# Kernel optimization log

Hardware: AMD Instinct MI355X
Metric: run time of the kernel (lower is better)

Reference implementation:

```python
import jax, jax.numpy as jnp
import numpy as np

EPS = 1e-5
K = 20  # hardcoded neighborhood size in get_graph_feature / get_neighbors


def _bn(x, p):
    # inference-mode BatchNorm; p = [gamma, beta, running_mean, running_var], channel axis = 1
    g, b, m, v = p
    sh = (1, -1) + (1,) * (x.ndim - 2)
    return (x - m.reshape(sh)) * (g.reshape(sh) / jnp.sqrt(v.reshape(sh) + EPS)) + b.reshape(sh)


def _knn(x, k):
    # x: [B, C, N] -> idx [B, N, k] of nearest neighbors (argmax of -squared-distance)
    xx = jnp.sum(x * x, axis=1)                       # [B, N]
    d = 2.0 * jnp.einsum('bcn,bcm->bnm', x, x) - xx[:, :, None] - xx[:, None, :]
    return jax.lax.top_k(d, k)[1]


def _gather(x, idx):
    # x: [B, C, N], idx: [B, N, k] -> [B, N, k, C]
    xt = jnp.transpose(x, (0, 2, 1))
    b = jnp.arange(x.shape[0])[:, None, None]
    return xt[b, idx]


def _graph_feature(x, k):
    # EdgeConv feature: cat(neighbor, center, center - neighbor) -> [B, 3C, N, k]
    nb = _gather(x, _knn(x, k))                                   # [B, N, k, C]
    xe = jnp.broadcast_to(jnp.transpose(x, (0, 2, 1))[:, :, None, :], nb.shape)
    feat = jnp.concatenate([nb, xe, xe - nb], axis=3)
    return jnp.transpose(feat, (0, 3, 1, 2))


def _att_pool(x, bn_p, w, b):
    # x: [B, C, N, K]; softmax attention over neighbor axis, weighted sum -> [B, C, N]
    h = jax.nn.relu(_bn(x, bn_p))
    att = jnp.einsum('oc,bcnk->bonk', w, h) + b[None, :, None, None]
    return jnp.sum(x * jax.nn.softmax(att, axis=-1), axis=-1)


def _lafe(x, w1, b1, w2, b2, w3, b3):
    # local_attention_extration; x: [B, 3, N] -> [B, 16, N]
    nb = _gather(x, _knn(x, K))                                   # [B, N, K, 3]
    xc = jnp.broadcast_to(jnp.transpose(x, (0, 2, 1))[:, :, None, :], nb.shape)
    xn = xc - nb                                                  # center - neighbor
    nf = jnp.einsum('oc,bnkc->bnko', w1, xc) + b1                 # conv2d1 -> [B,N,K,16]
    sa = jnp.einsum('o,bnko->bnk', w3[0], nf) + b3[0]             # self attention logits
    ef = jnp.einsum('oc,bnkc->bnko', w2, xn) + b2                 # conv2d2 edge feature
    na = jnp.einsum('o,bnko->bnk', w3[0], ef) + b3[0]             # neighbor attention logits
    coefs = jax.nn.softmax(jax.nn.leaky_relu(sa + na, 0.01), axis=-1)  # [B,N,K]
    vals = jnp.einsum('bnk,bnko->bno', coefs, ef)                 # [B,N,16]
    return jnp.transpose(jax.nn.elu(vals), (0, 2, 1))             # [B,16,N]


def _mk_bn(key, c):
    k1, k2, k3, k4 = jax.random.split(key, 4)
    g = 1.0 + 0.1 * jax.random.normal(k1, (c,))
    be = 0.1 * jax.random.normal(k2, (c,))
    m = 0.1 * jax.random.normal(k3, (c,))
    v = jax.random.uniform(k4, (c,), minval=0.5, maxval=1.5)
    return jnp.stack([g, be, m, v])


def setup_inputs() -> dict:
    key = jax.random.key(0)
    ks = jax.random.split(key, 20)
    B, N, E = 8, 2048, 512
    s = 0.05
    inp = {
        'x': jax.random.normal(ks[0], (B, 3, N), dtype=jnp.float32),
        'la_w1': s * jax.random.normal(ks[1], (16, 3)),
        'la_b1': s * jax.random.normal(ks[2], (16,)),
        'la_w2': s * jax.random.normal(ks[3], (16, 3)),
        'la_b2': s * jax.random.normal(ks[4], (16,)),
        'la_w3': s * jax.random.normal(ks[5], (1, 16)),
        'la_b3': s * jax.random.normal(ks[6], (1,)),
        'mlp_w': s * jax.random.normal(ks[7], (256, 19)),
        'mlp_b': s * jax.random.normal(ks[8], (256,)),
        'mlp_bn': _mk_bn(ks[9], 256),
        'w1': s * jax.random.normal(ks[10], (64, 57)),
        'bn1': _mk_bn(ks[11], 64),
        'w2': s * jax.random.normal(ks[12], (256, 249)),
        'bn2': _mk_bn(ks[13], 256),
        'w3': s * jax.random.normal(ks[14], (E, 512)),
        'bn3': _mk_bn(ks[15], E),
        'p1_bn': _mk_bn(ks[16], 64),
        'p1_w': s * jax.random.normal(ks[17], (64, 64)),
        'p1_b': s * jax.random.normal(ks[17], (64,)),
        'p2_bn': _mk_bn(ks[18], 256),
        'p2_w': s * jax.random.normal(ks[19], (256, 256)),
        'p2_b': s * jax.random.normal(ks[19], (256,)),
    }
    return inp


def reference(x, la_w1, la_b1, la_w2, la_b2, la_w3, la_b3,
              mlp_w, mlp_b, mlp_bn, w1, bn1, w2, bn2, w3, bn3,
              p1_bn, p1_w, p1_b, p2_bn, p2_w, p2_b):
    # Feature_Extration.forward, x: [B, 3, N] -> [B, 512, N]
    xm = _lafe(x, la_w1, la_b1, la_w2, la_b2, la_w3, la_b3)        # [B,16,N]
    x_manet = jnp.concatenate([x, xm], axis=1)                     # [B,19,N]
    x_mlp = jax.nn.relu(_bn(jnp.einsum('oc,bcn->bon', mlp_w, x_manet)
                            + mlp_b[None, :, None], mlp_bn))       # [B,256,N]
    g1 = _graph_feature(x_manet, K)                                # [B,57,N,20]
    h1 = jax.nn.leaky_relu(_bn(jnp.einsum('oc,bcnk->bonk', w1, g1), bn1), 0.2)
    xp1 = _att_pool(h1, p1_bn, p1_w, p1_b)                         # [B,64,N]
    x_c1 = jnp.concatenate([x_manet, xp1], axis=1)                 # [B,83,N]
    g2 = _graph_feature(x_c1, K)                                   # [B,249,N,20]
    h2 = jax.nn.leaky_relu(_bn(jnp.einsum('oc,bcnk->bonk', w2, g2), bn2), 0.2)
    xp2 = _att_pool(h2, p2_bn, p2_w, p2_b)                         # [B,256,N]
    x_c2 = jnp.concatenate([x_mlp, xp2], axis=1)                   # [B,512,N]
    out = jax.nn.leaky_relu(_bn(jnp.einsum('oc,bcn->bon', w3, x_c2), bn3), 0.2)
    return out
```

## Files before the change

kernel.cpp:

```cpp
#include <hip/hip_runtime.h>
#include <hip/hip_bf16.h>
#include <math.h>

typedef __hip_bfloat16 bf16;
typedef unsigned short ushort16_t;
typedef unsigned int uint32;
typedef __attribute__((ext_vector_type(8))) short short8;
typedef __attribute__((ext_vector_type(4))) float floatx4;

#define BB 8
#define NN 2048
#define KK 20

#define O_XMAN  0
#define O_XC1   311296
#define O_XC2   1671168
#define O_IDX2  10059776
#define O_IDX3  10387456
#define O_MLPW  10715136
#define O_MLPSC 10720256
#define O_MLPSH 10720512
#define O_W1P   10720768
#define O_BN1SC 10724864
#define O_BN1SH 10724928
#define O_P1SC  10724992
#define O_P1SH  10725056
#define O_P1W   10725120
#define O_P1B   10729216
#define O_W2P   10729280
#define O_BN2SC 10794816
#define O_BN2SH 10795072
#define O_P2SC  10795328
#define O_P2SH  10795584
#define O_P2W   10795840
#define O_P2B   10861376
#define O_W3P   10861632
#define O_BN3SC 11123776
#define O_BN3SH 11124288
#define O_LA    11124800
#define O_FLAG  11124960
#define O_W2B16 11125760
#define O_P2W16 11162624

#define O_W1S16 O_W1P
#define O_W3S16 O_W3P
#define O_W1A3  11195392

#define O_HILO  O_XC2
#define O_XXQ   (O_XC2 + 2097152)
#define O_UV1   (O_XC2 + 2113536)

__device__ __forceinline__ float ldin(const void* p, int i, int f32) {
    return f32 ? ((const float*)p)[i]
               : __bfloat162float(((const bf16*)p)[i]);
}

__device__ __forceinline__ ushort16_t f2bf(float v) {
    union { bf16 h; ushort16_t u; } x; x.h = __float2bfloat16(v); return x.u;
}

__device__ __forceinline__ float bfbits2f(ushort16_t u) {
    union { uint32 i; float f; } c; c.i = ((uint32)u) << 16; return c.f;
}

__global__ void detect_kernel(const void* x, int* flag) {
    if (threadIdx.x == 0 && blockIdx.x == 0) {
        const unsigned short* u = (const unsigned short*)x;
        int bad = 0;
        for (int i = 0; i < 64; ++i) {
            int e = (u[i] >> 7) & 0xFF;
            if (e >= 0x86) bad++;
        }
        *flag = (bad > 0) ? 1 : 0;
    }
}

__global__ void prep_kernel(
    const void* la_w1, const void* la_b1, const void* la_w2, const void* la_b2,
    const void* la_w3, const void* la_b3,
    const void* mlp_w, const void* mlp_b, const void* mlp_bn,
    const void* w1, const void* bn1, const void* w2, const void* bn2,
    const void* w3, const void* bn3,
    const void* p1_bn, const void* p1_w, const void* p1_b,
    const void* p2_bn, const void* p2_w, const void* p2_b,
    float* ws)
{
    const int f32 = ((const int*)ws)[O_FLAG];
    int gid = blockIdx.x * blockDim.x + threadIdx.x;
    int gsz = gridDim.x * blockDim.x;

    for (int i = gid; i < 256*20; i += gsz) {
        int o = i / 20, c = i - o*20;
        ws[O_MLPW + i] = (c < 19) ? ldin(mlp_w, o*19 + c, f32) : 0.f;
    }
    for (int c = gid; c < 256; c += gsz) {
        float g = ldin(mlp_bn, c, f32), be = ldin(mlp_bn, 256+c, f32);
        float m = ldin(mlp_bn, 512+c, f32), vv = ldin(mlp_bn, 768+c, f32);
        float s = g / sqrtf(vv + 1e-5f);
        ws[O_MLPSC + c] = s;
        ws[O_MLPSH + c] = be + (ldin(mlp_b, c, f32) - m) * s;
    }
    for (int c = gid; c < 64; c += gsz) {
        float g = ldin(bn1, c, f32), be = ldin(bn1, 64+c, f32);
        float m = ldin(bn1, 128+c, f32), vv = ldin(bn1, 192+c, f32);
        float s = g / sqrtf(vv + 1e-5f);
        ws[O_BN1SC + c] = s; ws[O_BN1SH + c] = be - m*s;
        float g2 = ldin(p1_bn, c, f32), be2 = ldin(p1_bn, 64+c, f32);
        float m2 = ldin(p1_bn, 128+c, f32), vv2 = ldin(p1_bn, 192+c, f32);
        float s2 = g2 / sqrtf(vv2 + 1e-5f);
        ws[O_P1SC + c] = s2; ws[O_P1SH + c] = be2 - m2*s2;
    }
    for (int c = gid; c < 256; c += gsz) {
        float g = ldin(bn2, c, f32), be = ldin(bn2, 256+c, f32);
        float m = ldin(bn2, 512+c, f32), vv = ldin(bn2, 768+c, f32);
        float s = g / sqrtf(vv + 1e-5f);
        ws[O_BN2SC + c] = s; ws[O_BN2SH + c] = be - m*s;
        float g2 = ldin(p2_bn, c, f32), be2 = ldin(p2_bn, 256+c, f32);
        float m2 = ldin(p2_bn, 512+c, f32), vv2 = ldin(p2_bn, 768+c, f32);
        float s2 = g2 / sqrtf(vv2 + 1e-5f);
        ws[O_P2SC + c] = s2; ws[O_P2SH + c] = be2 - m2*s2;
        ws[O_P2B + c] = ldin(p2_b, c, f32);
    }
    {
        ushort16_t* w3s = (ushort16_t*)(ws + O_W3S16);
        for (int i = gid; i < 512*1024; i += gsz) {
            int o = i >> 10, kp = i & 1023;
            int c = kp >> 1, s = kp & 1;
            float v = ldin(w3, o*512 + c, f32);
            ushort16_t h = f2bf(v);
            w3s[i] = (s == 0) ? h : f2bf(v - bfbits2f(h));
        }
    }
    for (int c = gid; c < 512; c += gsz) {
        float g = ldin(bn3, c, f32), be = ldin(bn3, 512+c, f32);
        float m = ldin(bn3, 1024+c, f32), vv = ldin(bn3, 1536+c, f32);
        float s = g / sqrtf(vv + 1e-5f);
        ws[O_BN3SC + c] = s; ws[O_BN3SH + c] = be - m*s;
    }
    for (int i = gid; i < 48; i += gsz) ws[O_LA + i]       = ldin(la_w1, i, f32);
    for (int i = gid; i < 16; i += gsz) ws[O_LA + 48 + i]  = ldin(la_b1, i, f32);
    for (int i = gid; i < 48; i += gsz) ws[O_LA + 64 + i]  = ldin(la_w2, i, f32);
    for (int i = gid; i < 16; i += gsz) ws[O_LA + 112 + i] = ldin(la_b2, i, f32);
    for (int i = gid; i < 16; i += gsz) ws[O_LA + 128 + i] = ldin(la_w3, i, f32);
    if (gid == 0) ws[O_LA + 144] = ldin(la_b3, 0, f32);

    ushort16_t* w1s = (ushort16_t*)(ws + O_W1S16);
    for (int i = gid; i < 128*64; i += gsz) {
        int row = i >> 6, kp = i & 63;
        if (kp < 57) {
            int c = kp / 3, s = kp - c*3;
            int o = row & 63;
            float wnb = ldin(w1, o*57 + c, f32);
            float wce = ldin(w1, o*57 + 19 + c, f32);
            float wdf = ldin(w1, o*57 + 38 + c, f32);
            float v = (row < 64) ? (wnb - wdf) : (wce + wdf);
            ushort16_t h = f2bf(v); float r1 = v - bfbits2f(h);
            ushort16_t m = f2bf(r1); ushort16_t l = f2bf(r1 - bfbits2f(m));
            w1s[i] = (s==0) ? h : ((s==1) ? m : l);
        } else w1s[i] = 0;
    }
    ushort16_t* w1a3 = (ushort16_t*)(ws + O_W1A3);
    for (int i = gid; i < 3*64*192; i += gsz) {
        int t = i / (64*192), rem = i - t*64*192;
        int o = rem / 192, kp = rem - o*192;
        int c = kp / 3;
        float v = ldin(p1_w, o*64 + c, f32);
        ushort16_t h = f2bf(v); float r1 = v - bfbits2f(h);
        ushort16_t m = f2bf(r1); ushort16_t l = f2bf(r1 - bfbits2f(m));
        w1a3[i] = (t==0) ? h : ((t==1) ? m : l);
    }

    ushort16_t* a2b = (ushort16_t*)(ws + O_W2B16);
    for (int i = gid; i < 256*96; i += gsz) {
        int row = i / 96, c = i - row*96;
        float v = (c < 83) ? (ldin(w2, row*249 + c, f32) - ldin(w2, row*249 + 166 + c, f32)) : 0.f;
        a2b[i] = f2bf(v);
    }
    float* b2fT = ws + O_P2W;
    for (int i = gid; i < 84*256; i += gsz) {
        int c = i >> 8, row = i & 255;
        b2fT[i] = (c < 83) ? (ldin(w2, row*249 + 83 + c, f32) + ldin(w2, row*249 + 166 + c, f32)) : 0.f;
    }
    ushort16_t* pwb = (ushort16_t*)(ws + O_P2W16);
    for (int i = gid; i < 256*256; i += gsz) pwb[i] = f2bf(ldin(p2_w, i, f32));
}

__global__ __launch_bounds__(256) void xconv_kernel(const void* x, float* ws) {
    const int f32 = ((const int*)ws)[O_FLAG];
    int gid = blockIdx.x*256 + threadIdx.x;
    int b = gid / (3*NN), r = gid - b*3*NN;
    ws[O_XMAN + b*19*NN + r] = ldin(x, gid, f32);
}

__global__ __launch_bounds__(256) void xc1copy_kernel(float* ws) {
    int gid = blockIdx.x*256 + threadIdx.x;
    int b = gid / (19*NN), r = gid - b*19*NN;
    ws[O_XC1 + (size_t)b*83*NN + r] = ws[O_XMAN + gid];
}

template<int C, int CS, int KP>
__global__ void hilo_kernel(const float* feat, ushort16_t* out) {
    int b  = blockIdx.x & 7;
    int lb = blockIdx.x >> 3;
    int nb = gridDim.x >> 3;
    const float* fb = feat + (size_t)b*CS*NN;
    ushort16_t* ob = out + (size_t)b*NN*KP;
    for (int i = lb*blockDim.x + threadIdx.x; i < C*NN; i += nb*blockDim.x) {
        int c = i >> 11, n = i & (NN-1);
        float v = fb[(size_t)c*NN + n];
        ushort16_t h = f2bf(v);
        float r1 = v - bfbits2f(h);
        ushort16_t m = f2bf(r1);
        ushort16_t l = f2bf(r1 - bfbits2f(m));
        size_t base = (size_t)n*KP + 3*c;
        ob[base] = h; ob[base+1] = m; ob[base+2] = l;
    }
    constexpr int PAD = KP - 3*C;
    for (int i = lb*blockDim.x + threadIdx.x; i < NN*PAD; i += nb*blockDim.x) {
        int n = i / PAD, p = i - n*PAD;
        ob[(size_t)n*KP + 3*C + p] = 0;
    }
}

template<int C, int CS>
__global__ __launch_bounds__(256) void xx_kernel(const float* feat, float* xxg) {
    int gid = blockIdx.x*256 + threadIdx.x;
    int b = gid >> 11, n = gid & (NN-1);
    const float* fb = feat + (size_t)b*CS*NN;
    float s = 0.f;
    #pragma unroll
    for (int c = 0; c < C; ++c) { float v = fb[c*NN + n]; s += v*v; }
    xxg[gid] = s;
}

template<int C, int CS, int KP>
__global__ __launch_bounds__(512, 2) void knn_fused_kernel(
    const float* feat, const ushort16_t* hilo, const float* xxg, int* idxout)
{
    constexpr int KT = KP / 32;
    constexpr int ST = 2057;
    __shared__ float Dt[16 * ST];
    int tid = threadIdx.x;
    int b  = blockIdx.x & 7;
    int n0 = (blockIdx.x >> 3) << 4;
    int lane = tid & 63, wv = tid >> 6;
    int quad = lane >> 4, l15 = lane & 15;
    const float* fb = feat + (size_t)b * CS * NN;

    short8 Bh[KT], Bm[KT], Bl[KT];
    #pragma unroll
    for (int kt = 0; kt < KT; ++kt) {
        #pragma unroll
        for (int e = 0; e < 8; ++e) {
            int kp = kt*32 + quad*8 + e;
            int c = kp / 3;
            float v = (c < C) ? fb[(size_t)c*NN + n0 + l15] : 0.f;
            ushort16_t h = f2bf(v);
            float r1 = v - bfbits2f(h);
            ushort16_t m = f2bf(r1);
            ushort16_t l = f2bf(r1 - bfbits2f(m));
            Bh[kt][e] = (short)h; Bm[kt][e] = (short)m; Bl[kt][e] = (short)l;
        }
    }

    const ushort16_t* hb = hilo + (size_t)b * NN * KP;
    const float* xxb = xxg + b * NN;

    #pragma unroll
    for (int i = 0; i < 4; ++i) {
        int base = (wv*4 + i) * 64;
        floatx4 acc[4];
        #pragma unroll
        for (int st = 0; st < 4; ++st) {
            acc[st] = (floatx4){0.f,0.f,0.f,0.f};
            #pragma unroll
            for (int kt = 0; kt < KT; ++kt) {
                short8 a = *(const short8*)&hb[(size_t)(base + st*16 + l15)*KP + kt*32 + quad*8];
                acc[st] = __builtin_amdgcn_mfma_f32_16x16x32_bf16(a, Bh[kt], acc[st], 0, 0, 0);
                acc[st] = __builtin_amdgcn_mfma_f32_16x16x32_bf16(a, Bm[kt], acc[st], 0, 0, 0);
                acc[st] = __builtin_amdgcn_mfma_f32_16x16x32_bf16(a, Bl[kt], acc[st], 0, 0, 0);
            }
        }
        #pragma unroll
        for (int st = 0; st < 4; ++st) {
            #pragma unroll
            for (int r = 0; r < 4; ++r) {
                int cand = base + st*16 + quad*4 + r;
                Dt[l15*ST + cand] = 2.f*acc[st][r] - xxb[cand];
            }
        }
    }
    __syncthreads();

    int r0 = wv*2, r1 = wv*2 + 1;
    unsigned int basei = 2047u - (unsigned int)lane;
    unsigned int a0[32], a1[32];
    unsigned int dead0 = 0, dead1 = 0;
    unsigned long long p0 = 0, p1 = 0, p2 = 0;
    unsigned long long q0 = 0, q1 = 0, q2 = 0;
    #pragma unroll
    for (int j = 0; j < 32; ++j) {
        unsigned int u0 = __float_as_uint(Dt[r0*ST + j*64 + lane]);
        unsigned int u1 = __float_as_uint(Dt[r1*ST + j*64 + lane]);
        unsigned int o0 = u0 ^ (unsigned int)(((int)u0 >> 31) | 0x80000000);
        unsigned int o1 = u1 ^ (unsigned int)(((int)u1 >> 31) | 0x80000000);
        a0[j] = o0; a1[j] = o1;
        unsigned long long k0 = ((unsigned long long)o0 << 32) | (basei - j*64);
        unsigned long long k1 = ((unsigned long long)o1 << 32) | (basei - j*64);
        bool g00 = k0 > p0, g01 = k0 > p1, g02 = k0 > p2;
        p2 = g01 ? p1 : (g02 ? k0 : p2);
        p1 = g00 ? p0 : (g01 ? k0 : p1);
        p0 = g00 ? k0 : p0;
        bool g10 = k1 > q0, g11 = k1 > q1, g12 = k1 > q2;
        q2 = g11 ? q1 : (g12 ? k1 : q2);
        q1 = g10 ? q0 : (g11 ? k1 : q1);
        q0 = g10 ? k1 : q0;
    }
    int myg0 = 0, myg1 = 0;
    #pragma unroll 1
    for (int it = 0; it < KK; ++it) {
        unsigned long long b0 = p0, b1 = q0;
        #pragma unroll
        for (int sh = 1; sh < 64; sh <<= 1) {
            unsigned long long o0 = __shfl_xor(b0, sh);
            unsigned long long o1 = __shfl_xor(b1, sh);
            b0 = (o0 > b0) ? o0 : b0;
            b1 = (o1 > b1) ? o1 : b1;
        }
        if (lane == it) {
            myg0 = (int)(2047u - (unsigned int)b0);
            myg1 = (int)(2047u - (unsigned int)b1);
        }
        if (p0 == b0) {
            dead0 |= 1u << ((int)(basei - (unsigned int)b0) >> 6);
            p0 = p1; p1 = p2; p2 = 0;
        }
        if (q0 == b1) {
            dead1 |= 1u << ((int)(basei - (unsigned int)b1) >> 6);
            q0 = q1; q1 = q2; q2 = 0;
        }
        if (__any((p0 == 0ull) | (q0 == 0ull))) {
            if (p0 == 0ull) {
                unsigned long long t0 = 0, t1 = 0, t2 = 0;
                #pragma unroll
                for (int j = 0; j < 32; ++j) {
                    unsigned long long k = ((dead0 >> j) & 1u) ? 0ull
                        : (((unsigned long long)a0[j] << 32) | (basei - j*64));
                    bool g0 = k > t0, g1 = k > t1, g2 = k > t2;
                    t2 = g1 ? t1 : (g2 ? k : t2);
                    t1 = g0 ? t0 : (g1 ? k : t1);
                    t0 = g0 ? k : t0;
                }
                p0 = t0; p1 = t1; p2 = t2;
            }
            if (q0 == 0ull) {
                unsigned long long t0 = 0, t1 = 0, t2 = 0;
                #pragma unroll
                for (int j = 0; j < 32; ++j) {
                    unsigned long long k = ((dead1 >> j) & 1u) ? 0ull
                        : (((unsigned long long)a1[j] << 32) | (basei - j*64));
                    bool g0 = k > t0, g1 = k > t1, g2 = k > t2;
                    t2 = g1 ? t1 : (g2 ? k : t2);
                    t1 = g0 ? t0 : (g1 ? k : t1);
                    t0 = g0 ? k : t0;
                }
                q0 = t0; q1 = t1; q2 = t2;
            }
        }
    }
    if (lane < KK) {
        idxout[((size_t)(b*NN + n0 + r0))*KK + lane] = myg0;
        idxout[((size_t)(b*NN + n0 + r1))*KK + lane] = myg1;
    }
}

__global__ __launch_bounds__(256, 1) void lafe_att_kernel(float* ws, const int* idx) {
    __shared__ float xs0[NN], xs1[NN], xs2[NN];
    int tid = threadIdx.x;
    int b = blockIdx.x >> 3;
    int n = ((blockIdx.x & 7) << 8) + tid;
    float* xm = ws + O_XMAN + b*19*NN;
    for (int i = tid; i < NN; i += 256) {
        xs0[i] = xm[i]; xs1[i] = xm[NN + i]; xs2[i] = xm[2*NN + i];
    }
    __syncthreads();
    float a0 = xs0[n], a1 = xs1[n], a2 = xs2[n];
    int ti[KK];
    #pragma unroll
    for (int k = 0; k < KK; ++k) ti[k] = idx[(b*NN + n)*KK + k] & (NN-1);
    const float* wl = ws + O_LA;
    float sa = wl[144];
    #pragma unroll
    for (int o = 0; o < 16; ++o) {
        float nf = wl[o*3+0]*a0 + wl[o*3+1]*a1 + wl[o*3+2]*a2 + wl[48+o];
        sa += wl[128+o]*nf;
    }
    float lg[KK]; float mx = -3.0e38f;
    #pragma unroll
    for (int k = 0; k < KK; ++k) {
        int m = ti[k];
        float d0 = a0 - xs0[m], d1 = a1 - xs1[m], d2 = a2 - xs2[m];
        float na = wl[144];
        #pragma unroll
        for (int o = 0; o < 16; ++o) {
            float ef = wl[64+o*3+0]*d0 + wl[64+o*3+1]*d1 + wl[64+o*3+2]*d2 + wl[112+o];
            na += wl[128+o]*ef;
        }
        float t = sa + na;
        t = t > 0.f ? t : 0.01f*t;
        lg[k] = t; mx = fmaxf(mx, t);
    }
    float ssum = 0.f;
    #pragma unroll
    for (int k = 0; k < KK; ++k) { lg[k] = expf(lg[k] - mx); ssum += lg[k]; }
    float vals[16];
    #pragma unroll
    for (int o = 0; o < 16; ++o) vals[o] = 0.f;
    #pragma unroll
    for (int k = 0; k < KK; ++k) {
        float coef = lg[k] / ssum;
        int m = ti[k];
        float d0 = a0 - xs0[m], d1 = a1 - xs1[m], d2 = a2 - xs2[m];
        #pragma unroll
        for (int o = 0; o < 16; ++o) {
            float ef = wl[64+o*3+0]*d0 + wl[64+o*3+1]*d1 + wl[64+o*3+2]*d2 + wl[112+o];
            vals[o] += coef * ef;
        }
    }
    #pragma unroll
    for (int o = 0; o < 16; ++o) {
        float v = vals[o];
        xm[(3+o)*NN + n] = v > 0.f ? v : expm1f(v);
    }
}

__global__ void mlp_kernel(float* ws) {
    __shared__ __align__(16) float xv[20];
    int tid = threadIdx.x;
    int b = blockIdx.x & 7, n = blockIdx.x >> 3;
    if (tid < 20) xv[tid] = (tid < 19) ? ws[O_XMAN + b*19*NN + tid*NN + n] : 0.f;
    __syncthreads();
    const float* mw = ws + O_MLPW;
    float acc = 0.f;
    #pragma unroll
    for (int c4 = 0; c4 < 5; ++c4) {
        float4 w = *(const float4*)&mw[tid*20 + c4*4];
        float4 g = *(const float4*)&xv[c4*4];
        acc += w.x*g.x + w.y*g.y + w.z*g.z + w.w*g.w;
    }
    float v = acc * ws[O_MLPSC + tid] + ws[O_MLPSH + tid];
    ws[O_XC2 + b*512*NN + tid*NN + n] = fmaxf(v, 0.f);
}

__global__ __launch_bounds__(256, 2) void uv1_kernel(float* ws) {
    __shared__ float xt[19*64];
    int tid = threadIdx.x;
    int b = blockIdx.x & 7;
    int pn0 = (blockIdx.x >> 3) << 6;
    const float* fb = ws + O_XMAN + (size_t)b*19*NN;
    for (int i = tid; i < 19*64; i += 256) {
        int c = i >> 6, j = i & 63;
        xt[i] = fb[(size_t)c*NN + pn0 + j];
    }
    __syncthreads();
    int lane = tid & 63, wv = tid >> 6;
    int quad = lane >> 4, l15 = lane & 15;

    short8 X[3][4][2];
    #pragma unroll
    for (int nt = 0; nt < 4; ++nt) {
        int pt = nt*16 + l15;
        #pragma unroll
        for (int kt = 0; kt < 2; ++kt) {
            #pragma unroll
            for (int e = 0; e < 8; ++e) {
                int kp = kt*32 + quad*8 + e;
                int c = kp / 3;
                float v = (c < 19) ? xt[c*64 + pt] : 0.f;
                ushort16_t h = f2bf(v); float r1 = v - bfbits2f(h);
                ushort16_t m = f2bf(r1); ushort16_t l = f2bf(r1 - bfbits2f(m));
                X[0][nt][kt][e] = (short)h;
                X[1][nt][kt][e] = (short)m;
                X[2][nt][kt][e] = (short)l;
            }
        }
    }
    const ushort16_t* w1s = (const ushort16_t*)(ws + O_W1S16);
    floatx4 acc[2][4];
    #pragma unroll
    for (int rt = 0; rt < 2; ++rt)
        #pragma unroll
        for (int nt = 0; nt < 4; ++nt) acc[rt][nt] = (floatx4){0.f,0.f,0.f,0.f};
    #pragma unroll
    for (int pass = 0; pass < 3; ++pass) {
        #pragma unroll
        for (int kt = 0; kt < 2; ++kt) {
            int c0 = kt*32 + quad*8;
            short8 a[2];
            a[0] = *(const short8*)&w1s[(wv*32 + l15)*64 + c0];
            a[1] = *(const short8*)&w1s[(wv*32 + 16 + l15)*64 + c0];
            #pragma unroll
            for (int rt = 0; rt < 2; ++rt)
                #pragma unroll
                for (int nt = 0; nt < 4; ++nt)
                    acc[rt][nt] = __builtin_amdgcn_mfma_f32_16x16x32_bf16(a[rt], X[pass][nt][kt], acc[rt][nt], 0, 0, 0);
        }
    }
    float* uv1 = ws + O_UV1 + (size_t)b*NN*128;
    #pragma unroll
    for (int rt = 0; rt < 2; ++rt)
        #pragma unroll
        for (int nt = 0; nt < 4; ++nt) {
            int n = pn0 + nt*16 + l15;
            int r = wv*32 + rt*16 + quad*4;
            *(float4*)&uv1[(size_t)n*128 + r] =
                make_float4(acc[rt][nt][0], acc[rt][nt][1], acc[rt][nt][2], acc[rt][nt][3]);
        }
}

__global__ __launch_bounds__(256, 2) void edge1_kernel(float* ws, const int* idx) {
    constexpr int SW = 204;
    constexpr int ST = 65;
    __shared__ __align__(16) ushort16_t hrS[80*SW];
    __shared__ __align__(16) float attL[80*ST];
    __shared__ float vL[4*64];
    __shared__ float scalL[256];
    __shared__ float outL[64*5];
    __shared__ int idxL[80];

    int tid = threadIdx.x;
    int b  = blockIdx.x & 7;
    int n0 = (blockIdx.x >> 3) << 2;
    const float* uv1 = ws + O_UV1 + (size_t)b*NN*128;

    {
        int grp = tid >> 6, r6 = tid & 63;
        int off = grp==0 ? O_BN1SC : grp==1 ? O_BN1SH : grp==2 ? O_P1SC : O_P1SH;
        scalL[tid] = ws[off + r6];
        vL[tid] = uv1[(size_t)(n0 + grp)*128 + 64 + r6];
    }
    if (tid < 80) idxL[tid] = idx[(b*NN + n0 + tid/20)*KK + (tid%20)] & (NN-1);
    __syncthreads();

    {
        int rw = tid & 63, cg = tid >> 6;
        float s1 = scalL[rw], sh1 = scalL[64+rw], ps = scalL[128+rw], ph = scalL[192+rw];
        #pragma unroll 5
        for (int it = 0; it < 20; ++it) {
            int col = it*4 + cg;
            int p = col / 20;
            int j = idxL[col];
            float u = uv1[(size_t)j*128 + rw];
            float h1 = (u + vL[p*64+rw])*s1 + sh1;
            h1 = h1 > 0.f ? h1 : 0.2f*h1;
            float hv = h1*ps + ph;
            hv = hv > 0.f ? hv : 0.f;
            ushort16_t h = f2bf(hv); float r1 = hv - bfbits2f(h);
            ushort16_t m = f2bf(r1); ushort16_t l = f2bf(r1 - bfbits2f(m));
            hrS[col*SW + 3*rw + 0] = h;
            hrS[col*SW + 3*rw + 1] = m;
            hrS[col*SW + 3*rw + 2] = l;
        }
    }
    __syncthreads();

    int lane = tid & 63, wv = tid >> 6;
    int quad = lane >> 4, l15 = lane & 15;
    const ushort16_t* w1a3 = (const ushort16_t*)(ws + O_W1A3);
    floatx4 acc[5];
    #pragma unroll
    for (int mt = 0; mt < 5; ++mt) acc[mt] = (floatx4){0.f,0.f,0.f,0.f};
    #pragma unroll
    for (int pass = 0; pass < 3; ++pass) {
        #pragma unroll
        for (int kt = 0; kt < 6; ++kt) {
            int c0 = kt*32 + quad*8;
            short8 bfrag = *(const short8*)&w1a3[((size_t)pass*64 + wv*16 + l15)*192 + c0];
            #pragma unroll
            for (int mt = 0; mt < 5; ++mt) {
                short8 afrag = *(const short8*)&hrS[(mt*16 + l15)*SW + c0];
                acc[mt] = __builtin_amdgcn_mfma_f32_16x16x32_bf16(afrag, bfrag, acc[mt], 0, 0, 0);
            }
        }
    }
    #pragma unroll
    for (int mt = 0; mt < 5; ++mt)
        #pragma unroll
        for (int r = 0; r < 4; ++r)
            attL[(mt*16 + quad*4 + r)*ST + wv*16 + l15] = acc[mt][r];
    __syncthreads();

    {
        int o = tid & 63, p = tid >> 6;
        float av[KK]; float mx = -3.0e38f;
        #pragma unroll
        for (int k = 0; k < KK; ++k) { av[k] = attL[(p*20 + k)*ST + o]; mx = fmaxf(mx, av[k]); }
        float ssum = 0.f;
        #pragma unroll
        for (int k = 0; k < KK; ++k) { av[k] = expf(av[k] - mx); ssum += av[k]; }
        float inv = 1.f / ssum;
        float s1o = scalL[o], sh1o = scalL[64+o], vpo = vL[p*64+o];
        float sacc = 0.f;
        #pragma unroll
        for (int k = 0; k < KK; ++k) {
            int j = idxL[p*20 + k];
            float u = uv1[(size_t)j*128 + o];
            float h1 = (u + vpo)*s1o + sh1o;
            h1 = h1 > 0.f ? h1 : 0.2f*h1;
            sacc += av[k]*inv*h1;
        }
        outL[o*5 + p] = sacc;
    }
    __syncthreads();
    {
        int o = tid >> 2, p = tid & 3;
        ws[O_XC1 + (size_t)b*83*NN + (size_t)(19+o)*NN + n0 + p] = outL[o*5 + p];
    }
}

__global__ __launch_bounds__(256, 2) void uv2_kernel(float* ws) {
    constexpr int XS = 108;
    __shared__ ushort16_t xt[64*XS];
    int tid = threadIdx.x;
    int b = blockIdx.x & 7;
    int pn0 = (blockIdx.x >> 3) << 6;
    const float* xc1 = ws + O_XC1 + (size_t)b*83*NN;
    for (int i = tid; i < 96*64; i += 256) {
        int c = i >> 6, j = i & 63;
        xt[j*XS + c] = (c < 83) ? f2bf(xc1[c*NN + pn0 + j]) : (ushort16_t)0;
    }
    __syncthreads();
    int lane = tid & 63, wv = tid >> 6;
    int quad = lane >> 4, l15 = lane & 15;
    const ushort16_t* a2b = (const ushort16_t*)(ws + O_W2B16);
    floatx4 acc[4][4];
    #pragma unroll
    for (int rt = 0; rt < 4; ++rt)
        #pragma unroll
        for (int nt = 0; nt < 4; ++nt) acc[rt][nt] = (floatx4){0.f,0.f,0.f,0.f};
    #pragma unroll
    for (int kt = 0; kt < 3; ++kt) {
        int c0 = kt*32 + quad*8;
        short8 bfr[4], a[4];
        #pragma unroll
        for (int nt = 0; nt < 4; ++nt)
            bfr[nt] = *(const short8*)&xt[(nt*16 + l15)*XS + c0];
        #pragma unroll
        for (int rt = 0; rt < 4; ++rt)
            a[rt] = *(const short8*)&a2b[(wv*64 + rt*16 + l15)*96 + c0];
        #pragma unroll
        for (int rt = 0; rt < 4; ++rt)
            #pragma unroll
            for (int nt = 0; nt < 4; ++nt)
                acc[rt][nt] = __builtin_amdgcn_mfma_f32_16x16x32_bf16(a[rt], bfr[nt], acc[rt][nt], 0, 0, 0);
    }
    float* U2 = ws + O_XC2 + (size_t)b*512*NN;
    #pragma unroll
    for (int rt = 0; rt < 4; ++rt)
        #pragma unroll
        for (int nt = 0; nt < 4; ++nt) {
            int n = pn0 + nt*16 + l15;
            int r = wv*64 + rt*16 + quad*4;
            *(float4*)&U2[(size_t)n*256 + r] =
                make_float4(acc[rt][nt][0], acc[rt][nt][1], acc[rt][nt][2], acc[rt][nt][3]);
        }
}

__global__ __launch_bounds__(256, 4) void v2_kernel(float* ws) {
    __shared__ float xs[83*16];
    int tid = threadIdx.x;
    int b = blockIdx.x & 7;
    int pn0 = (blockIdx.x >> 3) << 4;
    const float* xc1 = ws + O_XC1 + (size_t)b*83*NN;
    for (int i = tid; i < 83*16; i += 256) {
        int c = i >> 4, j = i & 15;
        xs[i] = xc1[(size_t)c*NN + pn0 + j];
    }
    __syncthreads();
    const float* b2fT = ws + O_P2W;
    float acc[16];
    #pragma unroll
    for (int j = 0; j < 16; ++j) acc[j] = 0.f;
    #pragma unroll 4
    for (int c = 0; c < 83; ++c) {
        float w = b2fT[c*256 + tid];
        #pragma unroll
        for (int j = 0; j < 16; ++j) acc[j] += w * xs[c*16 + j];
    }
    float* V2 = ws + O_XC2 + (size_t)b*512*NN + (size_t)256*NN;
    #pragma unroll
    for (int j = 0; j < 16; ++j) V2[(size_t)(pn0 + j)*256 + tid] = acc[j];
}

__global__ __launch_bounds__(256, 2) void edge2_kernel(float* ws, const int* idx) {
    constexpr int HS = 268;
    __shared__ __align__(16) ushort16_t hrb[48*HS];
    __shared__ __align__(16) float attL[256*41];
    __shared__ float p2bL[256];
    __shared__ int idxL[40];

    int tid = threadIdx.x;
    int b  = blockIdx.x & 7;
    int n0 = (blockIdx.x >> 3) << 1;

    const float* U2 = ws + O_XC2 + (size_t)b*512*NN;
    float* V2 = ws + O_XC2 + (size_t)b*512*NN + (size_t)256*NN;

    float sc = ws[O_BN2SC + tid], sh = ws[O_BN2SH + tid];
    float ps = ws[O_P2SC + tid],  ph = ws[O_P2SH + tid];
    p2bL[tid] = ws[O_P2B + tid];
    float v0 = V2[(size_t)n0*256 + tid];
    float v1 = V2[(size_t)(n0+1)*256 + tid];
    if (tid < 40) idxL[tid] = idx[(b*NN + n0 + tid/20)*KK + (tid%20)] & (NN-1);
    __syncthreads();

    float h2r[40];
    #pragma unroll
    for (int col = 0; col < 40; ++col) {
        int j = idxL[col];
        float u = U2[(size_t)j*256 + tid];
        float h2 = (u + (col >= 20 ? v1 : v0))*sc + sh;
        h2 = h2 > 0.f ? h2 : 0.2f*h2;
        h2r[col] = h2;
        float hv = h2*ps + ph;
        hrb[col*HS + tid] = f2bf(fmaxf(hv, 0.f));
    }
    __syncthreads();

    int lane = tid & 63, wv = tid >> 6;
    int quad = lane >> 4, l15 = lane & 15;
    const ushort16_t* p2wb = (const ushort16_t*)(ws + O_P2W16);
    floatx4 acc2[4][3];
    #pragma unroll
    for (int mt = 0; mt < 4; ++mt)
        #pragma unroll
        for (int nt = 0; nt < 3; ++nt) acc2[mt][nt] = (floatx4){0.f,0.f,0.f,0.f};
    for (int kt = 0; kt < 8; ++kt) {
        int c0 = kt*32 + quad*8;
        short8 a[4], bb3[3];
        #pragma unroll
        for (int mt = 0; mt < 4; ++mt)
            a[mt] = *(const short8*)&p2wb[(wv*64 + mt*16 + l15)*256 + c0];
        #pragma unroll
        for (int nt = 0; nt < 3; ++nt)
            bb3[nt] = *(const short8*)&hrb[(nt*16 + l15)*HS + c0];
        #pragma unroll
        for (int mt = 0; mt < 4; ++mt)
            #pragma unroll
            for (int nt = 0; nt < 3; ++nt)
                acc2[mt][nt] = __builtin_amdgcn_mfma_f32_16x16x32_bf16(a[mt], bb3[nt], acc2[mt][nt], 0, 0, 0);
    }
    #pragma unroll
    for (int mt = 0; mt < 4; ++mt) {
        int k0 = wv*64 + mt*16 + quad*4;
        #pragma unroll
        for (int nt = 0; nt < 3; ++nt) {
            int col = nt*16 + l15;
            if (col < 40) {
                #pragma unroll
                for (int r = 0; r < 4; ++r)
                    attL[(k0 + r)*41 + col] = acc2[mt][nt][r] + p2bL[k0 + r];
            }
        }
    }
    __syncthreads();

    #pragma unroll
    for (int p = 0; p < 2; ++p) {
        float av[KK]; float mx = -3.0e38f;
        #pragma unroll
        for (int k = 0; k < KK; ++k) { av[k] = attL[tid*41 + p*20 + k]; mx = fmaxf(mx, av[k]); }
        float ssum = 0.f;
        #pragma unroll
        for (int k = 0; k < KK; ++k) { av[k] = expf(av[k] - mx); ssum += av[k]; }
        float inv = 1.f / ssum;
        float sacc = 0.f;
        #pragma unroll
        for (int k = 0; k < KK; ++k) sacc += av[k] * inv * h2r[p*20 + k];
        V2[(size_t)(n0 + p)*256 + tid] = sacc;
    }
}

__global__ __launch_bounds__(512, 1) void final_kernel(const float* ws, float* out) {
    __shared__ __align__(16) uint32 smem[17408];
    __shared__ float s3L[512], q3L[512];
    uint32* xh32 = smem;
    uint32* xm32 = smem + 8448;
    float*  outF = (float*)smem;

    int tid = threadIdx.x;
    int b = blockIdx.x & 7;
    int pn0 = (blockIdx.x >> 3) << 6;
    int lane = tid & 63, wv = tid >> 6;
    int quad = lane >> 4, l15 = lane & 15;
    if (tid < 512) { s3L[tid] = ws[O_BN3SC + tid]; q3L[tid] = ws[O_BN3SH + tid]; }

    const float* xc2 = ws + O_XC2 + (size_t)b*512*NN;
    const float* xp2 = xc2 + (size_t)256*NN;
    const ushort16_t* w3s = (const ushort16_t*)(ws + O_W3S16);
    int r0 = wv*64;

    floatx4 acc[4][4];
    #pragma unroll
    for (int mt = 0; mt < 4; ++mt)
        #pragma unroll
        for (int nt = 0; nt < 4; ++nt) acc[mt][nt] = (floatx4){0.f,0.f,0.f,0.f};

    for (int ch = 0; ch < 4; ++ch) {
        __syncthreads();
        if (ch < 2) {
            int gc0 = ch*128;
            #pragma unroll 4
            for (int it = 0; it < 16; ++it) {
                int idx = it*512 + tid;
                int cl = idx >> 6, n = idx & 63;
                float v = xc2[(size_t)(gc0+cl)*NN + pn0 + n];
                ushort16_t h = f2bf(v);
                ushort16_t m = f2bf(v - bfbits2f(h));
                xh32[n*132 + cl] = (uint32)h * 0x10001u;
                xm32[n*132 + cl] = (uint32)m * 0x10001u;
            }
        } else {
            int gco = (ch-2)*128;
            #pragma unroll 4
            for (int it = 0; it < 16; ++it) {
                int idx = it*512 + tid;
                int n = idx >> 7, cl = idx & 127;
                float v = xp2[(size_t)(pn0+n)*256 + gco + cl];
                ushort16_t h = f2bf(v);
                ushort16_t m = f2bf(v - bfbits2f(h));
                xh32[n*132 + cl] = (uint32)h * 0x10001u;
                xm32[n*132 + cl] = (uint32)m * 0x10001u;
            }
        }
        __syncthreads();
        const ushort16_t* ph = (const ushort16_t*)xh32;
        const ushort16_t* pm = (const ushort16_t*)xm32;
        #pragma unroll
        for (int kt = 0; kt < 8; ++kt) {
            int c0k = kt*32 + quad*8;
            short8 a[4], bh[4], bm[4];
            #pragma unroll
            for (int mt = 0; mt < 4; ++mt)
                a[mt] = *(const short8*)&w3s[(size_t)(r0 + mt*16 + l15)*1024 + ch*256 + c0k];
            #pragma unroll
            for (int nt = 0; nt < 4; ++nt) {
                bh[nt] = *(const short8*)&ph[(nt*16 + l15)*264 + c0k];
                bm[nt] = *(const short8*)&pm[(nt*16 + l15)*264 + c0k];
            }
            #pragma unroll
            for (int mt = 0; mt < 4; ++mt)
                #pragma unroll
                for (int nt = 0; nt < 4; ++nt) {
                    acc[mt][nt] = __builtin_amdgcn_mfma_f32_16x16x32_bf16(a[mt], bh[nt], acc[mt][nt], 0, 0, 0);
                    acc[mt][nt] = __builtin_amdgcn_mfma_f32_16x16x32_bf16(a[mt], bm[nt], acc[mt][nt], 0, 0, 0);
                }
        }
    }

    float* ob = out + (size_t)b*512*NN;
    #pragma unroll
    for (int half = 0; half < 2; ++half) {
        __syncthreads();
        if ((wv >> 2) == half) {
            int rb = r0 - half*256;
            #pragma unroll
            for (int mt = 0; mt < 4; ++mt)
                #pragma unroll
                for (int nt = 0; nt < 4; ++nt)
                    #pragma unroll
                    for (int r = 0; r < 4; ++r) {
                        int row = r0 + mt*16 + quad*4 + r;
                        float v = acc[mt][nt][r]*s3L[row] + q3L[row];
                        v = v > 0.f ? v : 0.2f*v;
                        outF[(rb + mt*16 + quad*4 + r)*68 + nt*16 + l15] = v;
                    }
        }
        __syncthreads();
        #pragma unroll
        for (int it = 0; it < 8; ++it) {
            int idx = it*512 + tid;
            int row = idx >> 4, f4 = idx & 15;
            float4 v = *(const float4*)&outF[row*68 + f4*4];
            *(float4*)&ob[(size_t)(half*256 + row)*NN + pn0 + f4*4] = v;
        }
    }
}

extern "C" void kernel_launch(void* const* d_in, const int* in_sizes, int n_in,
                              void* d_out, int out_size, void* d_ws, size_t ws_size,
                              hipStream_t stream) {
    float* ws = (float*)d_ws;
    float* out = (float*)d_out;
    ushort16_t* hilo = (ushort16_t*)(ws + O_HILO);
    float* xxq = ws + O_XXQ;

    detect_kernel<<<1, 64, 0, stream>>>(d_in[0], (int*)ws + O_FLAG);
    prep_kernel<<<64, 256, 0, stream>>>(d_in[1], d_in[2], d_in[3], d_in[4], d_in[5], d_in[6],
                                        d_in[7], d_in[8], d_in[9], d_in[10], d_in[11], d_in[12],
                                        d_in[13], d_in[14], d_in[15], d_in[16], d_in[17], d_in[18],
                                        d_in[19], d_in[20], d_in[21], ws);
    xconv_kernel<<<192, 256, 0, stream>>>(d_in[0], ws);
    hilo_kernel<3, 19, 32><<<256, 256, 0, stream>>>(ws + O_XMAN, hilo);
    xx_kernel<3, 19><<<64, 256, 0, stream>>>(ws + O_XMAN, xxq);
    knn_fused_kernel<3, 19, 32><<<1024, 512, 0, stream>>>(ws + O_XMAN, hilo, xxq, (int*)(ws + O_IDX3));
    lafe_att_kernel<<<64, 256, 0, stream>>>(ws, (const int*)(ws + O_IDX3));
    xc1copy_kernel<<<1216, 256, 0, stream>>>(ws);
    hilo_kernel<19, 19, 64><<<1024, 256, 0, stream>>>(ws + O_XMAN, hilo);
    xx_kernel<19, 19><<<64, 256, 0, stream>>>(ws + O_XMAN, xxq);
    knn_fused_kernel<19, 19, 64><<<1024, 512, 0, stream>>>(ws + O_XMAN, hilo, xxq, (int*)(ws + O_IDX2));
    uv1_kernel<<<256, 256, 0, stream>>>(ws);
    edge1_kernel<<<BB*512, 256, 0, stream>>>(ws, (const int*)(ws + O_IDX2));
    hilo_kernel<83, 83, 256><<<2048, 256, 0, stream>>>(ws + O_XC1, hilo);
    xx_kernel<83, 83><<<64, 256, 0, stream>>>(ws + O_XC1, xxq);
    knn_fused_kernel<83, 83, 256><<<1024, 512, 0, stream>>>(ws + O_XC1, hilo, xxq, (int*)(ws + O_IDX3));
    uv2_kernel<<<256, 256, 0, stream>>>(ws);
    v2_kernel<<<1024, 256, 0, stream>>>(ws);
    edge2_kernel<<<BB*1024, 256, 0, stream>>>(ws, (const int*)(ws + O_IDX3));
    mlp_kernel<<<BB*NN, 256, 0, stream>>>(ws);
    final_kernel<<<256, 512, 0, stream>>>(ws, out);
}
```

Before: 1.008 ms.

## Double KNN block size to one query row per wave

The fused KNN kernel now runs 1024 threads per block (16 waves) instead of 512. Each wave computes two 64-candidate tiles instead of four and selects top-k for one query row instead of two. For large channel counts, the bf16 hi/mid/lo B fragments are built in two chunks so fewer are held in registers at once. The aim is more waves per CU, since the 131KB LDS tile allows only one block per CU, and less serial work per wave. The tighter launch bound risks register spills.

```diff
diff --git a/kernel.cpp b/kernel.cpp
--- a/kernel.cpp
+++ b/kernel.cpp
@@ -234,10 +234,12 @@
 }
 
 template<int C, int CS, int KP>
-__global__ __launch_bounds__(512, 2) void knn_fused_kernel(
+__global__ __launch_bounds__(1024, 4) void knn_fused_kernel(
     const float* feat, const ushort16_t* hilo, const float* xxg, int* idxout)
 {
     constexpr int KT = KP / 32;
+    constexpr int NCH = (KT > 4) ? 2 : 1;
+    constexpr int KTC = KT / NCH;
     constexpr int ST = 2057;
     __shared__ float Dt[16 * ST];
     int tid = threadIdx.x;
@@ -246,100 +248,92 @@
     int lane = tid & 63, wv = tid >> 6;
     int quad = lane >> 4, l15 = lane & 15;
     const float* fb = feat + (size_t)b * CS * NN;
-
-    short8 Bh[KT], Bm[KT], Bl[KT];
-    #pragma unroll
-    for (int kt = 0; kt < KT; ++kt) {
-        #pragma unroll
-        for (int e = 0; e < 8; ++e) {
-            int kp = kt*32 + quad*8 + e;
-            int c = kp / 3;
-            float v = (c < C) ? fb[(size_t)c*NN + n0 + l15] : 0.f;
-            ushort16_t h = f2bf(v);
-            float r1 = v - bfbits2f(h);
-            ushort16_t m = f2bf(r1);
-            ushort16_t l = f2bf(r1 - bfbits2f(m));
-            Bh[kt][e] = (short)h; Bm[kt][e] = (short)m; Bl[kt][e] = (short)l;
-        }
-    }
-
     const ushort16_t* hb = hilo + (size_t)b * NN * KP;
     const float* xxb = xxg + b * NN;
 
-    #pragma unroll
-    for (int i = 0; i < 4; ++i) {
-        int base = (wv*4 + i) * 64;
-        floatx4 acc[4];
+    floatx4 acc[2][4];
+    #pragma unroll
+    for (int i = 0; i < 2; ++i)
+        #pragma unroll
+        for (int st = 0; st < 4; ++st) acc[i][st] = (floatx4){0.f,0.f,0.f,0.f};
+
+    #pragma unroll
+    for (int ch = 0; ch < NCH; ++ch) {
+        short8 Bh[KTC], Bm[KTC], Bl[KTC];
+        #pragma unroll
+        for (int ktc = 0; ktc < KTC; ++ktc) {
+            #pragma unroll
+            for (int e = 0; e < 8; ++e) {
+                int kp = (ch*KTC + ktc)*32 + quad*8 + e;
+                int c = kp / 3;
+                float v = (c < C) ? fb[(size_t)c*NN + n0 + l15] : 0.f;
+                ushort16_t h = f2bf(v);
+                float r1 = v - bfbits2f(h);
+                ushort16_t m = f2bf(r1);
+                ushort16_t l = f2bf(r1 - bfbits2f(m));
+                Bh[ktc][e] = (short)h; Bm[ktc][e] = (short)m; Bl[ktc][e] = (short)l;
+            }
+        }
+        #pragma unroll
+        for (int i = 0; i < 2; ++i) {
+            int base = (wv*2 + i) * 64;
+            #pragma unroll
+            for (int st = 0; st < 4; ++st) {
+                #pragma unroll
+                for (int ktc = 0; ktc < KTC; ++ktc) {
+                    int kt = ch*KTC + ktc;
+                    short8 a = *(const short8*)&hb[(size_t)(base + st*16 + l15)*KP + kt*32 + quad*8];
+                    acc[i][st] = __builtin_amdgcn_mfma_f32_16x16x32_bf16(a, Bh[ktc], acc[i][st], 0, 0, 0);
+                    acc[i][st] = __builtin_amdgcn_mfma_f32_16x16x32_bf16(a, Bm[ktc], acc[i][st], 0, 0, 0);
+                    acc[i][st] = __builtin_amdgcn_mfma_f32_16x16x32_bf16(a, Bl[ktc], acc[i][st], 0, 0, 0);
+                }
+            }
+        }
+    }
+    #pragma unroll
+    for (int i = 0; i < 2; ++i) {
         #pragma unroll
         for (int st = 0; st < 4; ++st) {
-            acc[st] = (floatx4){0.f,0.f,0.f,0.f};
-            #pragma unroll
-            for (int kt = 0; kt < KT; ++kt) {
-                short8 a = *(const short8*)&hb[(size_t)(base + st*16 + l15)*KP + kt*32 + quad*8];
-                acc[st] = __builtin_amdgcn_mfma_f32_16x16x32_bf16(a, Bh[kt], acc[st], 0, 0, 0);
-                acc[st] = __builtin_amdgcn_mfma_f32_16x16x32_bf16(a, Bm[kt], acc[st], 0, 0, 0);
-                acc[st] = __builtin_amdgcn_mfma_f32_16x16x32_bf16(a, Bl[kt], acc[st], 0, 0, 0);
+            #pragma unroll
+            for (int r = 0; r < 4; ++r) {
+                int cand = (wv*2 + i)*64 + st*16 + quad*4 + r;
+                Dt[l15*ST + cand] = 2.f*acc[i][st][r] - xxb[cand];
             }
         }
-        #pragma unroll
-        for (int st = 0; st < 4; ++st) {
-            #pragma unroll
-            for (int r = 0; r < 4; ++r) {
-                int cand = base + st*16 + quad*4 + r;
-                Dt[l15*ST + cand] = 2.f*acc[st][r] - xxb[cand];
-            }
-        }
-    }
-    __syncthreads();
-
-    int r0 = wv*2, r1 = wv*2 + 1;
+    }
+    __syncthreads();
+
+    int r0 = wv;
     unsigned int basei = 2047u - (unsigned int)lane;
-    unsigned int a0[32], a1[32];
-    unsigned int dead0 = 0, dead1 = 0;
+    unsigned int a0[32];
+    unsigned int dead0 = 0;
     unsigned long long p0 = 0, p1 = 0, p2 = 0;
-    unsigned long long q0 = 0, q1 = 0, q2 = 0;
     #pragma unroll
     for (int j = 0; j < 32; ++j) {
         unsigned int u0 = __float_as_uint(Dt[r0*ST + j*64 + lane]);
-        unsigned int u1 = __float_as_uint(Dt[r1*ST + j*64 + lane]);
         unsigned int o0 = u0 ^ (unsigned int)(((int)u0 >> 31) | 0x80000000);
-        unsigned int o1 = u1 ^ (unsigned int)(((int)u1 >> 31) | 0x80000000);
-        a0[j] = o0; a1[j] = o1;
+        a0[j] = o0;
         unsigned long long k0 = ((unsigned long long)o0 << 32) | (basei - j*64);
-        unsigned long long k1 = ((unsigned long long)o1 << 32) | (basei - j*64);
         bool g00 = k0 > p0, g01 = k0 > p1, g02 = k0 > p2;
         p2 = g01 ? p1 : (g02 ? k0 : p2);
         p1 = g00 ? p0 : (g01 ? k0 : p1);
         p0 = g00 ? k0 : p0;
-        bool g10 = k1 > q0, g11 = k1 > q1, g12 = k1 > q2;
-        q2 = g11 ? q1 : (g12 ? k1 : q2);
-        q1 = g10 ? q0 : (g11 ? k1 : q1);
-        q0 = g10 ? k1 : q0;
-    }
-    int myg0 = 0, myg1 = 0;
+    }
+    int myg0 = 0;
     #pragma unroll 1
     for (int it = 0; it < KK; ++it) {
-        unsigned long long b0 = p0, b1 = q0;
+        unsigned long long b0 = p0;
         #pragma unroll
         for (int sh = 1; sh < 64; sh <<= 1) {
             unsigned long long o0 = __shfl_xor(b0, sh);
-            unsigned long long o1 = __shfl_xor(b1, sh);
             b0 = (o0 > b0) ? o0 : b0;
-            b1 = (o1 > b1) ? o1 : b1;
-        }
-        if (lane == it) {
-            myg0 = (int)(2047u - (unsigned int)b0);
-            myg1 = (int)(2047u - (unsigned int)b1);
-        }
+        }
+        if (lane == it) myg0 = (int)(2047u - (unsigned int)b0);
         if (p0 == b0) {
             dead0 |= 1u << ((int)(basei - (unsigned int)b0) >> 6);
             p0 = p1; p1 = p2; p2 = 0;
         }
-        if (q0 == b1) {
-            dead1 |= 1u << ((int)(basei - (unsigned int)b1) >> 6);
-            q0 = q1; q1 = q2; q2 = 0;
-        }
-        if (__any((p0 == 0ull) | (q0 == 0ull))) {
+        if (__any(p0 == 0ull)) {
             if (p0 == 0ull) {
                 unsigned long long t0 = 0, t1 = 0, t2 = 0;
                 #pragma unroll
@@ -353,25 +347,10 @@
                 }
                 p0 = t0; p1 = t1; p2 = t2;
             }
-            if (q0 == 0ull) {
-                unsigned long long t0 = 0, t1 = 0, t2 = 0;
-                #pragma unroll
-                for (int j = 0; j < 32; ++j) {
-                    unsigned long long k = ((dead1 >> j) & 1u) ? 0ull
-                        : (((unsigned long long)a1[j] << 32) | (basei - j*64));
-                    bool g0 = k > t0, g1 = k > t1, g2 = k > t2;
-                    t2 = g1 ? t1 : (g2 ? k : t2);
-                    t1 = g0 ? t0 : (g1 ? k : t1);
-                    t0 = g0 ? k : t0;
-                }
-                q0 = t0; q1 = t1; q2 = t2;
-            }
-        }
-    }
-    if (lane < KK) {
+        }
+    }
+    if (lane < KK)
         idxout[((size_t)(b*NN + n0 + r0))*KK + lane] = myg0;
-        idxout[((size_t)(b*NN + n0 + r1))*KK + lane] = myg1;
-    }
 }
 
 __global__ __launch_bounds__(256, 1) void lafe_att_kernel(float* ws, const int* idx) {
@@ -903,17 +882,17 @@
     xconv_kernel<<<192, 256, 0, stream>>>(d_in[0], ws);
     hilo_kernel<3, 19, 32><<<256, 256, 0, stream>>>(ws + O_XMAN, hilo);
     xx_kernel<3, 19><<<64, 256, 0, stream>>>(ws + O_XMAN, xxq);
-    knn_fused_kernel<3, 19, 32><<<1024, 512, 0, stream>>>(ws + O_XMAN, hilo, xxq, (int*)(ws + O_IDX3));
+    knn_fused_kernel<3, 19, 32><<<1024, 1024, 0, stream>>>(ws + O_XMAN, hilo, xxq, (int*)(ws + O_IDX3));
     lafe_att_kernel<<<64, 256, 0, stream>>>(ws, (const int*)(ws + O_IDX3));
     xc1copy_kernel<<<1216, 256, 0, stream>>>(ws);
     hilo_kernel<19, 19, 64><<<1024, 256, 0, stream>>>(ws + O_XMAN, hilo);
     xx_kernel<19, 19><<<64, 256, 0, stream>>>(ws + O_XMAN, xxq);
-    knn_fused_kernel<19, 19, 64><<<1024, 512, 0, stream>>>(ws + O_XMAN, hilo, xxq, (int*)(ws + O_IDX2));
+    knn_fused_kernel<19, 19, 64><<<1024, 1024, 0, stream>>>(ws + O_XMAN, hilo, xxq, (int*)(ws + O_IDX2));
     uv1_kernel<<<256, 256, 0, stream>>>(ws);
     edge1_kernel<<<BB*512, 256, 0, stream>>>(ws, (const int*)(ws + O_IDX2));
     hilo_kernel<83, 83, 256><<<2048, 256, 0, stream>>>(ws + O_XC1, hilo);
     xx_kernel<83, 83><<<64, 256, 0, stream>>>(ws + O_XC1, xxq);
-    knn_fused_kernel<83, 83, 256><<<1024, 512, 0, stream>>>(ws + O_XC1, hilo, xxq, (int*)(ws + O_IDX3));
+    knn_fused_kernel<83, 83, 256><<<1024, 1024, 0, stream>>>(ws + O_XC1, hilo, xxq, (int*)(ws + O_IDX3));
     uv2_kernel<<<256, 256, 0, stream>>>(ws);
     v2_kernel<<<1024, 256, 0, stream>>>(ws);
     edge2_kernel<<<BB*1024, 256, 0, stream>>>(ws, (const int*)(ws + O_IDX3));
```

Result: faster. 977.2 us (-3.1%).
